# Kernel tuning notes

Measured on AMD Instinct MI355X. Metric: run time of the kernel, lower is better.

## Reference

```python
import jax, jax.numpy as jnp
import numpy as np

N, T, D = 64, 2048, 512
NEG = -1e9


def setup_inputs() -> dict:
    key = jax.random.key(0)
    k1, k2, k3, k4 = jax.random.split(key, 4)
    return {
        "query": jax.random.normal(k1, (N, D), dtype=jnp.float32),
        "key": jax.random.normal(k2, (T, N, D), dtype=jnp.float32),
        "value": jax.random.normal(k3, (T, N, D), dtype=jnp.float32),
        "lens": jax.random.randint(k4, (N,), 0, T, dtype=jnp.int64)
        if jax.config.jax_enable_x64 else jax.random.randint(k4, (N,), 0, T, dtype=jnp.int32),
    }


def reference(query, key, value, lens):
    # key/value: (T, N, D) -> (N, T, D)
    k = jnp.transpose(key, (1, 0, 2))
    v = jnp.transpose(value, (1, 0, 2))
    # energy: (N, T) = per-batch matvec key @ query
    energy = jnp.einsum('ntd,nd->nt', k, query)
    # length mask: positions >= lens are masked with -1e9 (as in masked_fill_)
    mask = jnp.arange(energy.shape[1])[None, :] >= lens[:, None]
    energy = jnp.where(mask, jnp.asarray(NEG, energy.dtype), energy)
    attention = jax.nn.softmax(energy, axis=1)
    # context: (N, D)
    context = jnp.einsum('nt,ntd->nd', attention, v)
    return context
```

## Files before the change

kernel.cpp:

```cpp
#include <hip/hip_runtime.h>
#include <math.h>

#define N_B 64
#define T_LEN 2048
#define D_DIM 512
#define NEG (-1e9f)

__device__ __forceinline__ float dot8(const float4& qa, const float4& qb,
                                      const float4& ka, const float4& kb) {
    return qa.x * ka.x + qa.y * ka.y + qa.z * ka.z + qa.w * ka.w
         + qb.x * kb.x + qb.y * kb.y + qb.z * kb.z + qb.w * kb.w;
}

__global__ __launch_bounds__(256) void attn_partial(
    const float* __restrict__ q,
    const float* __restrict__ key,
    const float* __restrict__ val,
    const int*   __restrict__ lens,
    float* __restrict__ m_ws,
    float* __restrict__ l_ws,
    float* __restrict__ o_ws,
    int C)
{
    const int c    = blockIdx.x;
    const int n    = blockIdx.y;
    const int tid  = threadIdx.x;
    const int wave = tid >> 6;
    const int lane = tid & 63;
    const int TC   = T_LEN / C;
    const int RW   = TC >> 2;
    const int t0   = c * TC;
    const int len_n = lens[n];
    const int d0   = 2 * tid;

    if (len_n > 0 && t0 >= len_n) {
        if (tid == 0) { m_ws[n * C + c] = -INFINITY; l_ws[n * C + c] = 0.0f; }
        *reinterpret_cast<float2*>(o_ws + ((size_t)n * C + c) * D_DIM + d0) =
            make_float2(0.0f, 0.0f);
        return;
    }

    __shared__ float acc_sm[4][D_DIM];
    __shared__ float ml_sm[4][2];

    const int    wstart  = t0 + wave * RW;
    const size_t rstride = (size_t)N_B * D_DIM;

    float acc[8];
    #pragma unroll
    for (int j = 0; j < 8; ++j) acc[j] = 0.0f;
    float m = -INFINITY, l = 0.0f;

    if (len_n == 0) {
        const float* vr = val + ((size_t)wstart * N_B + n) * D_DIM + 8 * lane;
        for (int i = 0; i < RW; ++i) {
            const float4 va = *reinterpret_cast<const float4*>(vr);
            const float4 vb = *reinterpret_cast<const float4*>(vr + 4);
            vr += rstride;
            acc[0] += va.x; acc[1] += va.y; acc[2] += va.z; acc[3] += va.w;
            acc[4] += vb.x; acc[5] += vb.y; acc[6] += vb.z; acc[7] += vb.w;
        }
        m = NEG;
        l = (float)RW;
    } else {
        int nact = len_n - wstart;
        if (nact > RW) nact = RW;
        if (nact > 0) {
            const float4* q4 = reinterpret_cast<const float4*>(
                q + (size_t)n * D_DIM) + 2 * lane;
            const float4 qa = q4[0];
            const float4 qb = q4[1];

            const float* kr = key + ((size_t)wstart * N_B + n) * D_DIM + 8 * lane;
            const float* vr = val + ((size_t)wstart * N_B + n) * D_DIM + 8 * lane;

            float4 ka = *reinterpret_cast<const float4*>(kr);
            float4 kb = *reinterpret_cast<const float4*>(kr + 4);
            float4 na = ka, nb = kb;

            for (int i = 0; i < nact; ++i) {
                const float4 va = *reinterpret_cast<const float4*>(vr);
                const float4 vb = *reinterpret_cast<const float4*>(vr + 4);
                vr += rstride;
                if (i + 1 < nact) {
                    na = *reinterpret_cast<const float4*>(kr + rstride);
                    nb = *reinterpret_cast<const float4*>(kr + rstride + 4);
                }
                kr += rstride;

                float e = dot8(qa, qb, ka, kb);
                #pragma unroll
                for (int off = 32; off; off >>= 1) e += __shfl_xor(e, off);

                if (e > m) {
                    const float sc = __expf(m - e);
                    l *= sc;
                    #pragma unroll
                    for (int j = 0; j < 8; ++j) acc[j] *= sc;
                    m = e;
                }
                const float p = __expf(e - m);
                l += p;
                acc[0] += p * va.x; acc[1] += p * va.y;
                acc[2] += p * va.z; acc[3] += p * va.w;
                acc[4] += p * vb.x; acc[5] += p * vb.y;
                acc[6] += p * vb.z; acc[7] += p * vb.w;

                ka = na; kb = nb;
            }
        }
    }

    *reinterpret_cast<float4*>(&acc_sm[wave][8 * lane]) =
        make_float4(acc[0], acc[1], acc[2], acc[3]);
    *reinterpret_cast<float4*>(&acc_sm[wave][8 * lane + 4]) =
        make_float4(acc[4], acc[5], acc[6], acc[7]);
    if (lane == 0) { ml_sm[wave][0] = m; ml_sm[wave][1] = l; }
    __syncthreads();

    const float m0 = ml_sm[0][0], m1 = ml_sm[1][0];
    const float m2 = ml_sm[2][0], m3 = ml_sm[3][0];
    const float M  = fmaxf(fmaxf(m0, m1), fmaxf(m2, m3));
    const float s0 = __expf(m0 - M), s1 = __expf(m1 - M);
    const float s2 = __expf(m2 - M), s3 = __expf(m3 - M);

    float2 r;
    r.x = s0 * acc_sm[0][d0]     + s1 * acc_sm[1][d0]
        + s2 * acc_sm[2][d0]     + s3 * acc_sm[3][d0];
    r.y = s0 * acc_sm[0][d0 + 1] + s1 * acc_sm[1][d0 + 1]
        + s2 * acc_sm[2][d0 + 1] + s3 * acc_sm[3][d0 + 1];
    *reinterpret_cast<float2*>(o_ws + ((size_t)n * C + c) * D_DIM + d0) = r;

    if (tid == 0) {
        m_ws[n * C + c] = M;
        l_ws[n * C + c] = s0 * ml_sm[0][1] + s1 * ml_sm[1][1]
                        + s2 * ml_sm[2][1] + s3 * ml_sm[3][1];
    }
}

__global__ __launch_bounds__(256) void attn_combine(
    const float* __restrict__ m_ws,
    const float* __restrict__ l_ws,
    const float* __restrict__ o_ws,
    float* __restrict__ out,
    int C)
{
    const int n   = blockIdx.x;
    const int d   = blockIdx.y * 256 + threadIdx.x;
    const int tid = threadIdx.x;

    __shared__ float s_sm[64];
    __shared__ float S_sm;

    if (tid < 64) {
        const float m = (tid < C) ? m_ws[n * C + tid] : -INFINITY;
        float M = m;
        #pragma unroll
        for (int off = 32; off; off >>= 1) M = fmaxf(M, __shfl_xor(M, off));
        const float s = (tid < C) ? __expf(m - M) : 0.0f;
        s_sm[tid] = s;
        float S = s * ((tid < C) ? l_ws[n * C + tid] : 0.0f);
        #pragma unroll
        for (int off = 32; off; off >>= 1) S += __shfl_xor(S, off);
        if (tid == 0) S_sm = S;
    }
    __syncthreads();

    const float inv = 1.0f / S_sm;
    float acc = 0.0f;
    const float* op = o_ws + (size_t)n * C * D_DIM + d;
    for (int c = 0; c < C; ++c) {
        const float s = s_sm[c];
        if (s != 0.0f) acc += s * op[(size_t)c * D_DIM];
    }
    out[(size_t)n * D_DIM + d] = acc * inv;
}

extern "C" void kernel_launch(void* const* d_in, const int* in_sizes, int n_in,
                              void* d_out, int out_size, void* d_ws, size_t ws_size,
                              hipStream_t stream) {
    const float* q    = (const float*)d_in[0];
    const float* key  = (const float*)d_in[1];
    const float* val  = (const float*)d_in[2];
    const int*   lens = (const int*)d_in[3];
    float*       out  = (float*)d_out;

    int C = 32;
    while (C > 4 && (size_t)N_B * C * (D_DIM + 2) * sizeof(float) > ws_size) C >>= 1;

    float* m_ws = (float*)d_ws;
    float* l_ws = m_ws + (size_t)N_B * C;
    float* o_ws = l_ws + (size_t)N_B * C;

    attn_partial<<<dim3(C, N_B), 256, 0, stream>>>(q, key, val, lens,
                                                   m_ws, l_ws, o_ws, C);
    attn_combine<<<dim3(N_B, D_DIM / 256), 256, 0, stream>>>(m_ws, l_ws, o_ws,
                                                             out, C);
}
```

Before: 67.29 us.

## Compact active chunks into a work list and use persistent blocks with atomic scheduling

A new setup kernel resets the m/l workspace, counts the (batch, chunk) pairs that fall inside each sequence length, prefix-sums the counts and writes a compact work list. The partial kernel becomes persistent with 1024 blocks that pull items from that list through an atomic counter, so no blocks are launched for fully masked chunks and load is balanced across CUs. The cost is an extra single-block launch, an atomic plus two barriers per item, and serial list building in one wave. Skipped chunks leave o_ws unwritten, but combine never reads them because their weight is zero.

```diff
diff --git a/kernel.cpp b/kernel.cpp
--- a/kernel.cpp
+++ b/kernel.cpp
@@ -4,12 +4,54 @@
 #define N_B 64
 #define T_LEN 2048
 #define D_DIM 512
+#define C_CH 32
+#define TC (T_LEN / C_CH)
+#define RW (TC / 4)
 #define NEG (-1e9f)
+
 
 __device__ __forceinline__ float dot8(const float4& qa, const float4& qb,
                                       const float4& ka, const float4& kb) {
     return qa.x * ka.x + qa.y * ka.y + qa.z * ka.z + qa.w * ka.w
          + qb.x * kb.x + qb.y * kb.y + qb.z * kb.z + qb.w * kb.w;
+}
+
+__global__ __launch_bounds__(64) void attn_setup(
+    const int* __restrict__ lens,
+    int* __restrict__ ctl,
+    float* __restrict__ m_ws,
+    float* __restrict__ l_ws)
+{
+    const int tid = threadIdx.x;
+    for (int i = tid; i < N_B * C_CH; i += 64) {
+        m_ws[i] = -INFINITY;
+        l_ws[i] = 0.0f;
+    }
+    if (tid == 0) ctl[0] = 0;
+
+    int cnt = 0;
+    if (tid < C_CH) {
+        for (int n = 0; n < N_B; ++n) {
+            const int len = lens[n];
+            if (len == 0 || tid * TC < len) ++cnt;
+        }
+    }
+    int incl = cnt;
+    #pragma unroll
+    for (int off = 1; off < 64; off <<= 1) {
+        const int y = __shfl_up(incl, off);
+        if (tid >= off) incl += y;
+    }
+    const int base = incl - cnt;
+    if (tid == C_CH - 1) ctl[1] = incl;
+    if (tid < C_CH) {
+        int idx = base;
+        for (int n = 0; n < N_B; ++n) {
+            const int len = lens[n];
+            if (len == 0 || tid * TC < len)
+                ctl[2 + idx++] = (n << 8) | tid;
+        }
+    }
 }
 
 __global__ __launch_bounds__(256) void attn_partial(
@@ -17,124 +59,127 @@
     const float* __restrict__ key,
     const float* __restrict__ val,
     const int*   __restrict__ lens,
+    int*   __restrict__ ctl,
     float* __restrict__ m_ws,
     float* __restrict__ l_ws,
-    float* __restrict__ o_ws,
-    int C)
+    float* __restrict__ o_ws)
 {
-    const int c    = blockIdx.x;
-    const int n    = blockIdx.y;
     const int tid  = threadIdx.x;
     const int wave = tid >> 6;
     const int lane = tid & 63;
-    const int TC   = T_LEN / C;
-    const int RW   = TC >> 2;
-    const int t0   = c * TC;
-    const int len_n = lens[n];
     const int d0   = 2 * tid;
-
-    if (len_n > 0 && t0 >= len_n) {
-        if (tid == 0) { m_ws[n * C + c] = -INFINITY; l_ws[n * C + c] = 0.0f; }
-        *reinterpret_cast<float2*>(o_ws + ((size_t)n * C + c) * D_DIM + d0) =
-            make_float2(0.0f, 0.0f);
-        return;
-    }
+    const size_t rstride = (size_t)N_B * D_DIM;
+
+    const int total = ctl[1];
 
     __shared__ float acc_sm[4][D_DIM];
     __shared__ float ml_sm[4][2];
-
-    const int    wstart  = t0 + wave * RW;
-    const size_t rstride = (size_t)N_B * D_DIM;
-
-    float acc[8];
-    #pragma unroll
-    for (int j = 0; j < 8; ++j) acc[j] = 0.0f;
-    float m = -INFINITY, l = 0.0f;
-
-    if (len_n == 0) {
-        const float* vr = val + ((size_t)wstart * N_B + n) * D_DIM + 8 * lane;
-        for (int i = 0; i < RW; ++i) {
-            const float4 va = *reinterpret_cast<const float4*>(vr);
-            const float4 vb = *reinterpret_cast<const float4*>(vr + 4);
-            vr += rstride;
-            acc[0] += va.x; acc[1] += va.y; acc[2] += va.z; acc[3] += va.w;
-            acc[4] += vb.x; acc[5] += vb.y; acc[6] += vb.z; acc[7] += vb.w;
-        }
-        m = NEG;
-        l = (float)RW;
-    } else {
-        int nact = len_n - wstart;
-        if (nact > RW) nact = RW;
-        if (nact > 0) {
-            const float4* q4 = reinterpret_cast<const float4*>(
-                q + (size_t)n * D_DIM) + 2 * lane;
-            const float4 qa = q4[0];
-            const float4 qb = q4[1];
-
-            const float* kr = key + ((size_t)wstart * N_B + n) * D_DIM + 8 * lane;
+    __shared__ int   w_sm;
+
+    for (;;) {
+        __syncthreads();
+        if (tid == 0) w_sm = atomicAdd(&ctl[0], 1);
+        __syncthreads();
+        const int w = w_sm;
+        if (w >= total) break;
+
+        const int item  = ctl[2 + w];
+        const int n     = item >> 8;
+        const int c     = item & 255;
+        const int len_n = lens[n];
+        const int wstart = c * TC + wave * RW;
+
+        float acc[8];
+        #pragma unroll
+        for (int j = 0; j < 8; ++j) acc[j] = 0.0f;
+        float m = -INFINITY, l = 0.0f;
+
+        if (len_n == 0) {
             const float* vr = val + ((size_t)wstart * N_B + n) * D_DIM + 8 * lane;
-
-            float4 ka = *reinterpret_cast<const float4*>(kr);
-            float4 kb = *reinterpret_cast<const float4*>(kr + 4);
-            float4 na = ka, nb = kb;
-
-            for (int i = 0; i < nact; ++i) {
+            for (int i = 0; i < RW; ++i) {
                 const float4 va = *reinterpret_cast<const float4*>(vr);
                 const float4 vb = *reinterpret_cast<const float4*>(vr + 4);
                 vr += rstride;
-                if (i + 1 < nact) {
-                    na = *reinterpret_cast<const float4*>(kr + rstride);
-                    nb = *reinterpret_cast<const float4*>(kr + rstride + 4);
+                acc[0] += va.x; acc[1] += va.y; acc[2] += va.z; acc[3] += va.w;
+                acc[4] += vb.x; acc[5] += vb.y; acc[6] += vb.z; acc[7] += vb.w;
+            }
+            m = NEG;
+            l = (float)RW;
+        } else {
+            int nact = len_n - wstart;
+            if (nact > RW) nact = RW;
+            if (nact > 0) {
+                const float4* q4 = reinterpret_cast<const float4*>(
+                    q + (size_t)n * D_DIM) + 2 * lane;
+                const float4 qa = q4[0];
+                const float4 qb = q4[1];
+
+                const float* kr = key + ((size_t)wstart * N_B + n) * D_DIM + 8 * lane;
+                const float* vr = val + ((size_t)wstart * N_B + n) * D_DIM + 8 * lane;
+
+                float4 ka = *reinterpret_cast<const float4*>(kr);
+                float4 kb = *reinterpret_cast<const float4*>(kr + 4);
+                float4 na = ka, nb = kb;
+
+                for (int i = 0; i < nact; ++i) {
+                    const float4 va = *reinterpret_cast<const float4*>(vr);
+                    const float4 vb = *reinterpret_cast<const float4*>(vr + 4);
+                    vr += rstride;
+                    if (i + 1 < nact) {
+                        na = *reinterpret_cast<const float4*>(kr + rstride);
+                        nb = *reinterpret_cast<const float4*>(kr + rstride + 4);
+                    }
+                    kr += rstride;
+
+                    float e = dot8(qa, qb, ka, kb);
+                    #pragma unroll
+                    for (int off = 32; off; off >>= 1) e += __shfl_xor(e, off);
+
+                    if (e > m) {
+                        const float sc = __expf(m - e);
+                        l *= sc;
+                        #pragma unroll
+                        for (int j = 0; j < 8; ++j) acc[j] *= sc;
+                        m = e;
+                    }
+                    const float p = __expf(e - m);
+                    l += p;
+                    acc[0] += p * va.x; acc[1] += p * va.y;
+                    acc[2] += p * va.z; acc[3] += p * va.w;
+                    acc[4] += p * vb.x; acc[5] += p * vb.y;
+                    acc[6] += p * vb.z; acc[7] += p * vb.w;
+
+                    ka = na; kb = nb;
                 }
-                kr += rstride;
-
-                float e = dot8(qa, qb, ka, kb);
-                #pragma unroll
-                for (int off = 32; off; off >>= 1) e += __shfl_xor(e, off);
-
-                if (e > m) {
-                    const float sc = __expf(m - e);
-                    l *= sc;
-                    #pragma unroll
-                    for (int j = 0; j < 8; ++j) acc[j] *= sc;
-                    m = e;
-                }
-                const float p = __expf(e - m);
-                l += p;
-                acc[0] += p * va.x; acc[1] += p * va.y;
-                acc[2] += p * va.z; acc[3] += p * va.w;
-                acc[4] += p * vb.x; acc[5] += p * vb.y;
-                acc[6] += p * vb.z; acc[7] += p * vb.w;
-
-                ka = na; kb = nb;
             }
         }
-    }
-
-    *reinterpret_cast<float4*>(&acc_sm[wave][8 * lane]) =
-        make_float4(acc[0], acc[1], acc[2], acc[3]);
-    *reinterpret_cast<float4*>(&acc_sm[wave][8 * lane + 4]) =
-        make_float4(acc[4], acc[5], acc[6], acc[7]);
-    if (lane == 0) { ml_sm[wave][0] = m; ml_sm[wave][1] = l; }
-    __syncthreads();
-
-    const float m0 = ml_sm[0][0], m1 = ml_sm[1][0];
-    const float m2 = ml_sm[2][0], m3 = ml_sm[3][0];
-    const float M  = fmaxf(fmaxf(m0, m1), fmaxf(m2, m3));
-    const float s0 = __expf(m0 - M), s1 = __expf(m1 - M);
-    const float s2 = __expf(m2 - M), s3 = __expf(m3 - M);
-
-    float2 r;
-    r.x = s0 * acc_sm[0][d0]     + s1 * acc_sm[1][d0]
-        + s2 * acc_sm[2][d0]     + s3 * acc_sm[3][d0];
-    r.y = s0 * acc_sm[0][d0 + 1] + s1 * acc_sm[1][d0 + 1]
-        + s2 * acc_sm[2][d0 + 1] + s3 * acc_sm[3][d0 + 1];
-    *reinterpret_cast<float2*>(o_ws + ((size_t)n * C + c) * D_DIM + d0) = r;
-
-    if (tid == 0) {
-        m_ws[n * C + c] = M;
-        l_ws[n * C + c] = s0 * ml_sm[0][1] + s1 * ml_sm[1][1]
-                        + s2 * ml_sm[2][1] + s3 * ml_sm[3][1];
+
+        *reinterpret_cast<float4*>(&acc_sm[wave][8 * lane]) =
+            make_float4(acc[0], acc[1], acc[2], acc[3]);
+        *reinterpret_cast<float4*>(&acc_sm[wave][8 * lane + 4]) =
+            make_float4(acc[4], acc[5], acc[6], acc[7]);
+        if (lane == 0) { ml_sm[wave][0] = m; ml_sm[wave][1] = l; }
+        __syncthreads();
+
+        const float m0 = ml_sm[0][0], m1 = ml_sm[1][0];
+        const float m2 = ml_sm[2][0], m3 = ml_sm[3][0];
+        const float M  = fmaxf(fmaxf(m0, m1), fmaxf(m2, m3));
+        const float s0 = __expf(m0 - M), s1 = __expf(m1 - M);
+        const float s2 = __expf(m2 - M), s3 = __expf(m3 - M);
+
+        float2 r;
+        r.x = s0 * acc_sm[0][d0]     + s1 * acc_sm[1][d0]
+            + s2 * acc_sm[2][d0]     + s3 * acc_sm[3][d0];
+        r.y = s0 * acc_sm[0][d0 + 1] + s1 * acc_sm[1][d0 + 1]
+            + s2 * acc_sm[2][d0 + 1] + s3 * acc_sm[3][d0 + 1];
+        *reinterpret_cast<float2*>(
+            o_ws + ((size_t)n * C_CH + c) * D_DIM + d0) = r;
+
+        if (tid == 0) {
+            m_ws[n * C_CH + c] = M;
+            l_ws[n * C_CH + c] = s0 * ml_sm[0][1] + s1 * ml_sm[1][1]
+                               + s2 * ml_sm[2][1] + s3 * ml_sm[3][1];
+        }
     }
 }
 
@@ -142,8 +187,7 @@
     const float* __restrict__ m_ws,
     const float* __restrict__ l_ws,
     const float* __restrict__ o_ws,
-    float* __restrict__ out,
-    int C)
+    float* __restrict__ out)
 {
     const int n   = blockIdx.x;
     const int d   = blockIdx.y * 256 + threadIdx.x;
@@ -153,13 +197,13 @@
     __shared__ float S_sm;
 
     if (tid < 64) {
-        const float m = (tid < C) ? m_ws[n * C + tid] : -INFINITY;
+        const float m = (tid < C_CH) ? m_ws[n * C_CH + tid] : -INFINITY;
         float M = m;
         #pragma unroll
         for (int off = 32; off; off >>= 1) M = fmaxf(M, __shfl_xor(M, off));
-        const float s = (tid < C) ? __expf(m - M) : 0.0f;
+        const float s = (tid < C_CH) ? __expf(m - M) : 0.0f;
         s_sm[tid] = s;
-        float S = s * ((tid < C) ? l_ws[n * C + tid] : 0.0f);
+        float S = s * ((tid < C_CH) ? l_ws[n * C_CH + tid] : 0.0f);
         #pragma unroll
         for (int off = 32; off; off >>= 1) S += __shfl_xor(S, off);
         if (tid == 0) S_sm = S;
@@ -168,8 +212,8 @@
 
     const float inv = 1.0f / S_sm;
     float acc = 0.0f;
-    const float* op = o_ws + (size_t)n * C * D_DIM + d;
-    for (int c = 0; c < C; ++c) {
+    const float* op = o_ws + (size_t)n * C_CH * D_DIM + d;
+    for (int c = 0; c < C_CH; ++c) {
         const float s = s_sm[c];
         if (s != 0.0f) acc += s * op[(size_t)c * D_DIM];
     }
@@ -185,15 +229,14 @@
     const int*   lens = (const int*)d_in[3];
     float*       out  = (float*)d_out;
 
-    int C = 32;
-    while (C > 4 && (size_t)N_B * C * (D_DIM + 2) * sizeof(float) > ws_size) C >>= 1;
-
-    float* m_ws = (float*)d_ws;
-    float* l_ws = m_ws + (size_t)N_B * C;
-    float* o_ws = l_ws + (size_t)N_B * C;
-
-    attn_partial<<<dim3(C, N_B), 256, 0, stream>>>(q, key, val, lens,
-                                                   m_ws, l_ws, o_ws, C);
-    attn_combine<<<dim3(N_B, D_DIM / 256), 256, 0, stream>>>(m_ws, l_ws, o_ws,
-                                                             out, C);
-}
+    int*   ctl  = (int*)d_ws;
+    float* m_ws = (float*)((char*)d_ws + 16384);
+    float* l_ws = m_ws + N_B * C_CH;
+    float* o_ws = l_ws + N_B * C_CH;
+
+    attn_setup<<<1, 64, 0, stream>>>(lens, ctl, m_ws, l_ws);
+    attn_partial<<<1024, 256, 0, stream>>>(q, key, val, lens, ctl,
+                                           m_ws, l_ws, o_ws);
+    attn_combine<<<dim3(N_B, D_DIM / 256), 256, 0, stream>>>(m_ws, l_ws,
+                                                             o_ws, out);
+}
```

Result: slower. 85.62 us (+27.2%).
